# Performance work log

Hardware: AMD Instinct MI355X
Metric: run time of the kernel (lower is better)

The kernel has to match this reference:

```python
import jax, jax.numpy as jnp
import numpy as np

N, L, E, H = 8, 1024, 512, 4


def setup_inputs() -> dict:
    key = jax.random.key(0)
    ks = jax.random.split(key, 10)
    s = 1.0 / np.sqrt(E)
    return {
        "modalA": jax.random.normal(ks[0], (N, L, E), dtype=jnp.float32),
        "modalB": jax.random.normal(ks[1], (N, L, E), dtype=jnp.float32),
        "WqA": jax.random.normal(ks[2], (E, E), dtype=jnp.float32) * s,
        "bqA": jax.random.normal(ks[3], (E,), dtype=jnp.float32) * s,
        "WkA": jax.random.normal(ks[4], (E, E), dtype=jnp.float32) * s,
        "bkA": jax.random.normal(ks[5], (E,), dtype=jnp.float32) * s,
        "WqB": jax.random.normal(ks[6], (E, E), dtype=jnp.float32) * s,
        "bqB": jax.random.normal(ks[7], (E,), dtype=jnp.float32) * s,
        "WkB": jax.random.normal(ks[8], (E, E), dtype=jnp.float32) * s,
        "bkB": jax.random.normal(ks[9], (E,), dtype=jnp.float32) * s,
    }


def reference(modalA, modalB, WqA, bqA, WkA, bkA, WqB, bqB, WkB, bkB):
    # torch Linear: y = x @ W.T + b
    qA = modalA @ WqA.T + bqA  # [N, L, E]
    kA = modalA @ WkA.T + bkA
    qB = modalB @ WqB.T + bqB
    kB = modalB @ WkB.T + bkB

    # mean over heads of per-head dot products == full-dim dot / num_heads
    # (algebraically identical to einsum('nqhd,nkhd->nhqk').mean(1))
    inv_scale = 1.0 / (H * np.sqrt(E).astype(np.float32))

    def attn(q, k):
        scores = jnp.einsum('nqd,nkd->nqk', q, k) * inv_scale  # [N, L, L]
        return jax.nn.softmax(scores, axis=-1)

    weighted_A = attn(qA, kA)
    weighted_B = attn(qB, kB)
    weighted_AB = attn(qA, kB)
    weighted_BA = attn(qB, kA)

    cat_lower = jnp.concatenate([weighted_A, weighted_AB], axis=-1)  # [N, L, 2L]
    cat_upper = jnp.concatenate([weighted_B, weighted_BA], axis=-1)  # [N, L, 2L]
    cat = jnp.concatenate([cat_lower, cat_upper], axis=1)            # [N, 2L, 2L]
    return jnp.mean(cat, axis=0)                                     # [2L, 2L]
```

## Files before the change

kernel.cpp:

```cpp
#include <hip/hip_runtime.h>
#include <hip/hip_bf16.h>

typedef __bf16 bf16;
typedef bf16 bf16x8 __attribute__((ext_vector_type(8)));
typedef bf16 bf16x4v __attribute__((ext_vector_type(4)));
typedef _Float16 f16;
typedef f16 f16x4 __attribute__((ext_vector_type(4)));
typedef float f32x4 __attribute__((ext_vector_type(4)));

constexpr int LL = 1024;
constexpr int EE = 512;
constexpr int NBATCH = 8;

__device__ __forceinline__ f32x4 mfma16(bf16x8 a, bf16x8 b, f32x4 c) {
    return __builtin_amdgcn_mfma_f32_16x16x32_bf16(a, b, c, 0, 0, 0);
}

#define GLOAD_LDS16(g, l)                                                     \
    __builtin_amdgcn_global_load_lds(                                         \
        (const __attribute__((address_space(1))) void*)(g),                   \
        (__attribute__((address_space(3))) void*)(l), 16, 0, 0)

struct CvtParams {
    const float* src[6];
    bf16* dst[6];
    int n4[6];
};

__global__ __launch_bounds__(256) void cvt_kernel(CvtParams p) {
    const int y = blockIdx.y;
    const float* __restrict__ src = p.src[y];
    bf16* __restrict__ dst = p.dst[y];
    const int n4 = p.n4[y];
    for (int i = blockIdx.x * 256 + threadIdx.x; i < n4; i += gridDim.x * 256) {
        float4 v = *(const float4*)(src + (size_t)i * 4);
        bf16x4v o;
        o[0] = (bf16)v.x; o[1] = (bf16)v.y; o[2] = (bf16)v.z; o[3] = (bf16)v.w;
        *(bf16x4v*)(dst + (size_t)i * 4) = o;
    }
}

struct ProjParams {
    const bf16* x[4];
    const bf16* w[4];
    const float* b[4];
};

__global__ __launch_bounds__(256) void proj_kernel(ProjParams p, bf16* __restrict__ outbase) {
    const int z = blockIdx.z;
    const bf16* __restrict__ X = p.x[z];
    const bf16* __restrict__ W = p.w[z];
    const float* __restrict__ Bv = p.b[z];
    bf16* __restrict__ O = outbase + (size_t)z * (NBATCH * LL) * EE;

    __shared__ union {
        struct { alignas(16) bf16 A[128][32]; alignas(16) bf16 B[128][32]; } st;
        alignas(16) bf16 ep[128][140];
    } sm;

    const int t = threadIdx.x;
    const int lane = t & 63, wid = t >> 6;
    const int wm = wid & 1, wn = wid >> 1;
    const int lr = lane & 15, kg = lane >> 4;
    const int bx = blockIdx.x, by = blockIdx.y;

    f32x4 acc[4][4] = {};

    const int srow = t >> 2;
    const int scol = (t & 3) * 8;

    for (int k0 = 0; k0 < EE; k0 += 32) {
#pragma unroll
        for (int i = 0; i < 2; ++i) {
            const int r = srow + 64 * i;
            GLOAD_LDS16(X + (size_t)(by * 128 + r) * EE + k0 + scol, &sm.st.A[r][scol]);
            GLOAD_LDS16(W + (size_t)(bx * 128 + r) * EE + k0 + scol, &sm.st.B[r][scol]);
        }
        __builtin_amdgcn_s_waitcnt(0);
        __syncthreads();
        bf16x8 af[4], bfr[4];
#pragma unroll
        for (int im = 0; im < 4; ++im)
            af[im] = *(const bf16x8*)&sm.st.A[wm * 64 + im * 16 + lr][kg * 8];
#pragma unroll
        for (int in = 0; in < 4; ++in)
            bfr[in] = *(const bf16x8*)&sm.st.B[wn * 64 + in * 16 + lr][kg * 8];
#pragma unroll
        for (int im = 0; im < 4; ++im)
#pragma unroll
            for (int in = 0; in < 4; ++in)
                acc[im][in] = mfma16(af[im], bfr[in], acc[im][in]);
        __syncthreads();
    }

#pragma unroll
    for (int im = 0; im < 4; ++im) {
        const int row = wm * 64 + im * 16 + kg * 4;
#pragma unroll
        for (int in = 0; in < 4; ++in) {
            const int col = wn * 64 + in * 16 + lr;
            const float bias = Bv[bx * 128 + col];
#pragma unroll
            for (int r = 0; r < 4; ++r)
                sm.ep[row + r][col] = (bf16)(acc[im][in][r] + bias);
        }
    }
    __syncthreads();
#pragma unroll
    for (int i = 0; i < 8; ++i) {
        const int c = i * 256 + t;
        const int row = c >> 4, colg = (c & 15) * 8;
        *(uint4*)(O + (size_t)(by * 128 + row) * EE + bx * 128 + colg) =
            *(const uint4*)&sm.ep[row][colg];
    }
}

struct ScoresParams {
    const bf16* q[4];
    const bf16* k[4];
    f16* s[4];
};

__global__ __launch_bounds__(256) void scores_kernel(ScoresParams p) {
    const int map = blockIdx.z >> 3;
    const int n = blockIdx.z & 7;
    const bf16* __restrict__ Qb = p.q[map] + (size_t)n * LL * EE;
    const bf16* __restrict__ Kb = p.k[map] + (size_t)n * LL * EE;
    f16* __restrict__ Sb = p.s[map] + (size_t)n * LL * LL;

    __shared__ union {
        struct { alignas(16) bf16 A[128][32]; alignas(16) bf16 B[128][32]; } st;
        alignas(16) f16 ep[128][140];
    } sm;

    const int t = threadIdx.x;
    const int lane = t & 63, wid = t >> 6;
    const int wm = wid & 1, wn = wid >> 1;
    const int lr = lane & 15, kg = lane >> 4;
    const int bx = blockIdx.x, by = blockIdx.y;

    f32x4 acc[4][4] = {};

    const int srow = t >> 2;
    const int scol = (t & 3) * 8;

    for (int k0 = 0; k0 < EE; k0 += 32) {
#pragma unroll
        for (int i = 0; i < 2; ++i) {
            const int r = srow + 64 * i;
            GLOAD_LDS16(Qb + (size_t)(by * 128 + r) * EE + k0 + scol, &sm.st.A[r][scol]);
            GLOAD_LDS16(Kb + (size_t)(bx * 128 + r) * EE + k0 + scol, &sm.st.B[r][scol]);
        }
        __builtin_amdgcn_s_waitcnt(0);
        __syncthreads();
        bf16x8 af[4], bfr[4];
#pragma unroll
        for (int im = 0; im < 4; ++im)
            af[im] = *(const bf16x8*)&sm.st.A[wm * 64 + im * 16 + lr][kg * 8];
#pragma unroll
        for (int in = 0; in < 4; ++in)
            bfr[in] = *(const bf16x8*)&sm.st.B[wn * 64 + in * 16 + lr][kg * 8];
#pragma unroll
        for (int im = 0; im < 4; ++im)
#pragma unroll
            for (int in = 0; in < 4; ++in)
                acc[im][in] = mfma16(af[im], bfr[in], acc[im][in]);
        __syncthreads();
    }

    const float inv_scale = 0.011048543456039806f;
#pragma unroll
    for (int im = 0; im < 4; ++im) {
        const int row = wm * 64 + im * 16 + kg * 4;
#pragma unroll
        for (int in = 0; in < 4; ++in) {
            const int col = wn * 64 + in * 16 + lr;
#pragma unroll
            for (int r = 0; r < 4; ++r)
                sm.ep[row + r][col] = (f16)(acc[im][in][r] * inv_scale);
        }
    }
    __syncthreads();
#pragma unroll
    for (int i = 0; i < 8; ++i) {
        const int c = i * 256 + t;
        const int row = c >> 4, colg = (c & 15) * 8;
        *(uint4*)(Sb + (size_t)(by * 128 + row) * LL + bx * 128 + colg) =
            *(const uint4*)&sm.ep[row][colg];
    }
}

struct SmParams {
    const f16* s[4];
};

__global__ __launch_bounds__(256) void softmax_mean_kernel(SmParams p, float* __restrict__ out) {
    const int q = blockIdx.x;
    const int map = blockIdx.y;
    const f16* __restrict__ S = p.s[map];
    const int t = threadIdx.x;
    const int lane = t & 63, wid = t >> 6;
    __shared__ float red[NBATCH][4];

    f16x4 v[NBATCH];
#pragma unroll
    for (int n = 0; n < NBATCH; ++n)
        v[n] = *(const f16x4*)(S + ((size_t)n * LL + q) * LL + t * 4);

    float e[NBATCH][4];
#pragma unroll
    for (int n = 0; n < NBATCH; ++n) {
        float s = 0.f;
#pragma unroll
        for (int j = 0; j < 4; ++j) {
            e[n][j] = __expf((float)v[n][j]);
            s += e[n][j];
        }
#pragma unroll
        for (int off = 32; off; off >>= 1) s += __shfl_xor(s, off);
        if (lane == 0) red[n][wid] = s;
    }
    __syncthreads();

    float acc[4] = {};
#pragma unroll
    for (int n = 0; n < NBATCH; ++n) {
        const float inv = 1.0f / (red[n][0] + red[n][1] + red[n][2] + red[n][3]);
#pragma unroll
        for (int j = 0; j < 4; ++j) acc[j] += e[n][j] * inv;
    }

    const int orow = (map >= 2 ? LL : 0) + q;
    const int ocol = (map & 1 ? LL : 0) + t * 4;
    float4 o = make_float4(acc[0] * 0.125f, acc[1] * 0.125f, acc[2] * 0.125f, acc[3] * 0.125f);
    *(float4*)(out + (size_t)orow * (2 * LL) + ocol) = o;
}

extern "C" void kernel_launch(void* const* d_in, const int* in_sizes, int n_in,
                              void* d_out, int out_size, void* d_ws, size_t ws_size,
                              hipStream_t stream) {
    const float* modalA = (const float*)d_in[0];
    const float* modalB = (const float*)d_in[1];
    const float* WqA = (const float*)d_in[2];
    const float* bqA = (const float*)d_in[3];
    const float* WkA = (const float*)d_in[4];
    const float* bkA = (const float*)d_in[5];
    const float* WqB = (const float*)d_in[6];
    const float* bqB = (const float*)d_in[7];
    const float* WkB = (const float*)d_in[8];
    const float* bkB = (const float*)d_in[9];
    float* out = (float*)d_out;

    const size_t projN = (size_t)(NBATCH * LL) * EE;
    const size_t mapN = (size_t)NBATCH * LL * LL;
    char* base = (char*)d_ws;
    bf16* qk = (bf16*)base;
    char* region2 = base + 4 * projN * sizeof(bf16);
    bf16* XA = (bf16*)region2;
    bf16* XB = XA + projN;
    bf16* W4 = XB + projN;
    f16* S = (f16*)region2;

    CvtParams cp;
    cp.src[0] = modalA; cp.dst[0] = XA; cp.n4[0] = (int)(projN / 4);
    cp.src[1] = modalB; cp.dst[1] = XB; cp.n4[1] = (int)(projN / 4);
    const float* wsrc[4] = {WqA, WkA, WqB, WkB};
    for (int i = 0; i < 4; ++i) {
        cp.src[2 + i] = wsrc[i];
        cp.dst[2 + i] = W4 + (size_t)i * EE * EE;
        cp.n4[2 + i] = EE * EE / 4;
    }
    cvt_kernel<<<dim3(512, 6), 256, 0, stream>>>(cp);

    ProjParams pp;
    pp.x[0] = XA; pp.x[1] = XA; pp.x[2] = XB; pp.x[3] = XB;
    for (int i = 0; i < 4; ++i) pp.w[i] = W4 + (size_t)i * EE * EE;
    pp.b[0] = bqA; pp.b[1] = bkA; pp.b[2] = bqB; pp.b[3] = bkB;
    proj_kernel<<<dim3(4, 64, 4), 256, 0, stream>>>(pp, qk);

    const bf16* qA = qk + 0 * projN;
    const bf16* kA = qk + 1 * projN;
    const bf16* qB = qk + 2 * projN;
    const bf16* kB = qk + 3 * projN;

    ScoresParams sp;
    sp.q[0] = qA; sp.q[1] = qA; sp.q[2] = qB; sp.q[3] = qB;
    sp.k[0] = kA; sp.k[1] = kB; sp.k[2] = kB; sp.k[3] = kA;
    for (int m = 0; m < 4; ++m) sp.s[m] = S + (size_t)m * mapN;
    scores_kernel<<<dim3(8, 8, 32), 256, 0, stream>>>(sp);

    SmParams smp;
    for (int m = 0; m < 4; ++m) smp.s[m] = S + (size_t)m * mapN;
    softmax_mean_kernel<<<dim3(1024, 4), 256, 0, stream>>>(smp, out);
}
```

Baseline: 202.8 us.

## Swizzle LDS tiles, halve epilogue staging, and remap scores blocks per XCD

```diff
diff --git a/kernel.cpp b/kernel.cpp
--- a/kernel.cpp
+++ b/kernel.cpp
@@ -40,6 +40,7 @@
     }
 }
 
+
 struct ProjParams {
     const bf16* x[4];
     const bf16* w[4];
@@ -55,7 +56,7 @@
 
     __shared__ union {
         struct { alignas(16) bf16 A[128][32]; alignas(16) bf16 B[128][32]; } st;
-        alignas(16) bf16 ep[128][140];
+        alignas(16) bf16 ep[64][136];
     } sm;
 
     const int t = threadIdx.x;
@@ -67,24 +68,26 @@
     f32x4 acc[4][4] = {};
 
     const int srow = t >> 2;
-    const int scol = (t & 3) * 8;
+    const int cgl = t & 3;
+    const int gcg = (cgl ^ ((srow >> 1) & 3)) * 8;
+    const int scg = (kg ^ ((lr >> 1) & 3)) * 8;
 
     for (int k0 = 0; k0 < EE; k0 += 32) {
 #pragma unroll
         for (int i = 0; i < 2; ++i) {
             const int r = srow + 64 * i;
-            GLOAD_LDS16(X + (size_t)(by * 128 + r) * EE + k0 + scol, &sm.st.A[r][scol]);
-            GLOAD_LDS16(W + (size_t)(bx * 128 + r) * EE + k0 + scol, &sm.st.B[r][scol]);
+            GLOAD_LDS16(X + (size_t)(by * 128 + r) * EE + k0 + gcg, &sm.st.A[r][cgl * 8]);
+            GLOAD_LDS16(W + (size_t)(bx * 128 + r) * EE + k0 + gcg, &sm.st.B[r][cgl * 8]);
         }
         __builtin_amdgcn_s_waitcnt(0);
         __syncthreads();
         bf16x8 af[4], bfr[4];
 #pragma unroll
         for (int im = 0; im < 4; ++im)
-            af[im] = *(const bf16x8*)&sm.st.A[wm * 64 + im * 16 + lr][kg * 8];
+            af[im] = *(const bf16x8*)&sm.st.A[wm * 64 + im * 16 + lr][scg];
 #pragma unroll
         for (int in = 0; in < 4; ++in)
-            bfr[in] = *(const bf16x8*)&sm.st.B[wn * 64 + in * 16 + lr][kg * 8];
+            bfr[in] = *(const bf16x8*)&sm.st.B[wn * 64 + in * 16 + lr][scg];
 #pragma unroll
         for (int im = 0; im < 4; ++im)
 #pragma unroll
@@ -94,24 +97,30 @@
     }
 
 #pragma unroll
-    for (int im = 0; im < 4; ++im) {
-        const int row = wm * 64 + im * 16 + kg * 4;
-#pragma unroll
-        for (int in = 0; in < 4; ++in) {
-            const int col = wn * 64 + in * 16 + lr;
-            const float bias = Bv[bx * 128 + col];
-#pragma unroll
-            for (int r = 0; r < 4; ++r)
-                sm.ep[row + r][col] = (bf16)(acc[im][in][r] + bias);
-        }
-    }
-    __syncthreads();
-#pragma unroll
-    for (int i = 0; i < 8; ++i) {
-        const int c = i * 256 + t;
-        const int row = c >> 4, colg = (c & 15) * 8;
-        *(uint4*)(O + (size_t)(by * 128 + row) * EE + bx * 128 + colg) =
-            *(const uint4*)&sm.ep[row][colg];
+    for (int pph = 0; pph < 2; ++pph) {
+        if (wm == pph) {
+#pragma unroll
+            for (int im = 0; im < 4; ++im) {
+                const int row = im * 16 + kg * 4;
+#pragma unroll
+                for (int in = 0; in < 4; ++in) {
+                    const int col = wn * 64 + in * 16 + lr;
+                    const float bias = Bv[bx * 128 + col];
+#pragma unroll
+                    for (int r = 0; r < 4; ++r)
+                        sm.ep[row + r][col] = (bf16)(acc[im][in][r] + bias);
+                }
+            }
+        }
+        __syncthreads();
+#pragma unroll
+        for (int i = 0; i < 4; ++i) {
+            const int c = i * 256 + t;
+            const int row = c >> 4, colg = (c & 15) * 8;
+            *(uint4*)(O + (size_t)(by * 128 + pph * 64 + row) * EE + bx * 128 + colg) =
+                *(const uint4*)&sm.ep[row][colg];
+        }
+        __syncthreads();
     }
 }
 
@@ -122,44 +131,51 @@
 };
 
 __global__ __launch_bounds__(256) void scores_kernel(ScoresParams p) {
-    const int map = blockIdx.z >> 3;
-    const int n = blockIdx.z & 7;
+    const int f = blockIdx.x + (blockIdx.y << 3) + (blockIdx.z << 6);
+    const int xcd = f & 7;
+    const int j = f >> 3;
+    const int z = (xcd << 2) + (j >> 6);
+    const int map = z >> 3, n = z & 7;
+    const int tile = j & 63;
+    const int bx = tile & 7, by = tile >> 3;
+
     const bf16* __restrict__ Qb = p.q[map] + (size_t)n * LL * EE;
     const bf16* __restrict__ Kb = p.k[map] + (size_t)n * LL * EE;
     f16* __restrict__ Sb = p.s[map] + (size_t)n * LL * LL;
 
     __shared__ union {
         struct { alignas(16) bf16 A[128][32]; alignas(16) bf16 B[128][32]; } st;
-        alignas(16) f16 ep[128][140];
+        alignas(16) f16 ep[64][136];
     } sm;
 
     const int t = threadIdx.x;
     const int lane = t & 63, wid = t >> 6;
     const int wm = wid & 1, wn = wid >> 1;
     const int lr = lane & 15, kg = lane >> 4;
-    const int bx = blockIdx.x, by = blockIdx.y;
 
     f32x4 acc[4][4] = {};
 
     const int srow = t >> 2;
-    const int scol = (t & 3) * 8;
+    const int cgl = t & 3;
+    const int gcg = (cgl ^ ((srow >> 1) & 3)) * 8;
+    const int scg = (kg ^ ((lr >> 1) & 3)) * 8;
 
     for (int k0 = 0; k0 < EE; k0 += 32) {
 #pragma unroll
         for (int i = 0; i < 2; ++i) {
             const int r = srow + 64 * i;
-            GLOAD_LDS16(Qb + (size_t)(by * 128 + r) * EE + k0 + scol, &sm.st.A[r][scol]);
-            GLOAD_LDS16(Kb + (size_t)(bx * 128 + r) * EE + k0 + scol, &sm.st.B[r][scol]);
+            GLOAD_LDS16(Qb + (size_t)(by * 128 + r) * EE + k0 + gcg, &sm.st.A[r][cgl * 8]);
+            GLOAD_LDS16(Kb + (size_t)(bx * 128 + r) * EE + k0 + gcg, &sm.st.B[r][cgl * 8]);
         }
         __builtin_amdgcn_s_waitcnt(0);
         __syncthreads();
         bf16x8 af[4], bfr[4];
 #pragma unroll
         for (int im = 0; im < 4; ++im)
-            af[im] = *(const bf16x8*)&sm.st.A[wm * 64 + im * 16 + lr][kg * 8];
+            af[im] = *(const bf16x8*)&sm.st.A[wm * 64 + im * 16 + lr][scg];
 #pragma unroll
         for (int in = 0; in < 4; ++in)
-            bfr[in] = *(const bf16x8*)&sm.st.B[wn * 64 + in * 16 + lr][kg * 8];
+            bfr[in] = *(const bf16x8*)&sm.st.B[wn * 64 + in * 16 + lr][scg];
 #pragma unroll
         for (int im = 0; im < 4; ++im)
 #pragma unroll
@@ -170,23 +186,29 @@
 
     const float inv_scale = 0.011048543456039806f;
 #pragma unroll
-    for (int im = 0; im < 4; ++im) {
-        const int row = wm * 64 + im * 16 + kg * 4;
-#pragma unroll
-        for (int in = 0; in < 4; ++in) {
-            const int col = wn * 64 + in * 16 + lr;
-#pragma unroll
-            for (int r = 0; r < 4; ++r)
-                sm.ep[row + r][col] = (f16)(acc[im][in][r] * inv_scale);
-        }
-    }
-    __syncthreads();
-#pragma unroll
-    for (int i = 0; i < 8; ++i) {
-        const int c = i * 256 + t;
-        const int row = c >> 4, colg = (c & 15) * 8;
-        *(uint4*)(Sb + (size_t)(by * 128 + row) * LL + bx * 128 + colg) =
-            *(const uint4*)&sm.ep[row][colg];
+    for (int pph = 0; pph < 2; ++pph) {
+        if (wm == pph) {
+#pragma unroll
+            for (int im = 0; im < 4; ++im) {
+                const int row = im * 16 + kg * 4;
+#pragma unroll
+                for (int in = 0; in < 4; ++in) {
+                    const int col = wn * 64 + in * 16 + lr;
+#pragma unroll
+                    for (int r = 0; r < 4; ++r)
+                        sm.ep[row + r][col] = (f16)(acc[im][in][r] * inv_scale);
+                }
+            }
+        }
+        __syncthreads();
+#pragma unroll
+        for (int i = 0; i < 4; ++i) {
+            const int c = i * 256 + t;
+            const int row = c >> 4, colg = (c & 15) * 8;
+            *(uint4*)(Sb + (size_t)(by * 128 + pph * 64 + row) * LL + bx * 128 + colg) =
+                *(const uint4*)&sm.ep[row][colg];
+        }
+        __syncthreads();
     }
 }
 
```

After: 194.9 us. 3.9% less time.
